# Kernel tuning notes

Hardware: AMD Instinct MI355X
Metric: run time of the kernel (lower is better)

## Reference

```python
import jax, jax.numpy as jnp
import numpy as np

N_NODES = 100000
N_EDGES = 1000000
D_NODE = 64
D_EDGE = 32
D_OUT = 64
EPS = 1e-07
BETA = 1.0


def setup_inputs() -> dict:
    key = jax.random.key(0)
    ks = jax.random.split(key, 6)
    node_feats = jax.random.normal(ks[0], (N_NODES, D_NODE), dtype=jnp.float32)
    edge_feats = jax.random.normal(ks[1], (N_EDGES, D_EDGE), dtype=jnp.float32)
    src = jax.random.randint(ks[2], (N_EDGES,), 0, N_NODES, dtype=jnp.int32)
    dst = jax.random.randint(ks[3], (N_EDGES,), 0, N_NODES, dtype=jnp.int32)
    We = jax.random.normal(ks[4], (D_EDGE, D_OUT), dtype=jnp.float32) / np.sqrt(D_EDGE)
    be = jnp.zeros((D_OUT,), dtype=jnp.float32)
    Wm = jax.random.normal(ks[5], (D_NODE, D_OUT), dtype=jnp.float32) / np.sqrt(D_NODE)
    bm = jnp.zeros((D_OUT,), dtype=jnp.float32)
    return {"node_feats": node_feats, "edge_feats": edge_feats, "src": src,
            "dst": dst, "We": We, "be": be, "Wm": Wm, "bm": bm}


def reference(node_feats, edge_feats, src, dst, We, be, Wm, bm):
    n = node_feats.shape[0]
    # edge encoder + u_add_e: m_e = h_src + Linear(e)
    m = node_feats[src] + (edge_feats @ We + be)          # [E, D]
    m = jax.nn.relu(m) + EPS
    # segmented (per-destination) softmax over edges, per feature channel
    z = m * BETA
    zmax = jax.ops.segment_max(z, dst, num_segments=n)    # [N, D]
    ez = jnp.exp(z - zmax[dst])                           # [E, D]
    denom = jax.ops.segment_sum(ez, dst, num_segments=n)  # [N, D]
    a = ez / denom[dst]                                   # [E, D]
    # weighted scatter-sum aggregation
    agg = jax.ops.segment_sum(m * a, dst, num_segments=n) # [N, D]
    feats = node_feats + agg
    # mlp_layers=1 -> single Linear
    return feats @ Wm + bm
```

## Files before the change

kernel.cpp:

```cpp
#include <hip/hip_runtime.h>

#define D_NODE 64
#define D_EDGE 32
#define D_OUT  64
#define EPSF   1e-7f
#define CAP    48
#define CHUNK  8

typedef const __attribute__((address_space(1))) unsigned int guint_t;
typedef __attribute__((address_space(3))) unsigned int luint_t;
typedef float f32x2 __attribute__((ext_vector_type(2)));

__global__ __launch_bounds__(256) void genconv_build_kernel(
    const int* __restrict__ src,
    const int* __restrict__ dst,
    int* __restrict__ cnt,
    int2* __restrict__ slots,
    int E)
{
    const int e = blockIdx.x * blockDim.x + threadIdx.x;
    if (e >= E) return;
    const int d = dst[e];
    const int pos = atomicAdd(&cnt[d], 1);
    if (pos < CAP)
        slots[d * CAP + pos] = make_int2(e, src[e]);
}

__global__ __launch_bounds__(256) void genconv_gather_kernel(
    const float* __restrict__ node,
    const float* __restrict__ ef,
    const int*  __restrict__ cnt,
    const int2* __restrict__ slots,
    const float* __restrict__ We,
    const float* __restrict__ be,
    const float* __restrict__ Wm,
    const float* __restrict__ bm,
    float* __restrict__ out,
    int N)
{
    __shared__ float wm_s[D_NODE * D_OUT];
    __shared__ __align__(16) float efs[4][2][CHUNK * D_EDGE];
    __shared__ __align__(16) float fbuf[4][D_NODE];

    for (int i = threadIdx.x; i < D_NODE * D_OUT; i += blockDim.x)
        wm_s[i] = Wm[i];
    __syncthreads();

    const int lane  = (int)(threadIdx.x & 63);
    const int wslot = (int)(threadIdx.x >> 6);
    float* const efA    = efs[wslot][0];
    float* const efB    = efs[wslot][1];
    float* const fbuf_w = fbuf[wslot];

    f32x2 w2[D_EDGE / 2];
#pragma unroll
    for (int k2 = 0; k2 < D_EDGE / 2; ++k2) {
        w2[k2][0] = We[(2 * k2 + 0) * D_OUT + lane];
        w2[k2][1] = We[(2 * k2 + 1) * D_OUT + lane];
    }
    const float bias_e = be[lane];
    const float bias_m = bm[lane];

    const int wid = (int)((blockIdx.x * blockDim.x + threadIdx.x) >> 6);
    const int nw  = (int)((gridDim.x * blockDim.x) >> 6);

    int n = wid;
    int   c_pf   = 0;
    int2  sl_pf  = make_int2(0, 0);
    float res_pf = 0.0f;
    if (n < N) {
        c_pf   = cnt[n];
        sl_pf  = (lane < CAP) ? slots[n * CAP + lane] : make_int2(0, 0);
        res_pf = node[(size_t)n * D_NODE + lane];
    }

    struct HBank { float h0, h1, h2, h3, h4, h5, h6, h7; };

    while (n < N) {
        const int c = min(c_pf, CAP);
        const int e_l = (lane < c) ? sl_pf.x : 0;
        const int s_l = (lane < c) ? sl_pf.y : 0;
        const float fres = res_pf;

        const int n_next = n + nw;
        if (n_next < N) {
            c_pf   = cnt[n_next];
            sl_pf  = (lane < CAP) ? slots[n_next * CAP + lane] : make_int2(0, 0);
            res_pf = node[(size_t)n_next * D_NODE + lane];
        }
        __builtin_amdgcn_sched_barrier(0);

        float num = 0.0f, den = 0.0f;

        auto stage = [&](int base, float* dstLDS) {
            const int r  = base + (lane >> 3);
            const int er = __builtin_amdgcn_ds_bpermute(r << 2, e_l);
            const float* g = ef + (size_t)er * D_EDGE + ((lane & 7) << 2);
            __builtin_amdgcn_global_load_lds((guint_t*)g, (luint_t*)dstLDS, 16, 0, 0);
        };
        auto hload = [&](int base, HBank& H) {
            const int s0 = __builtin_amdgcn_readlane(s_l, base + 0);
            const int s1 = __builtin_amdgcn_readlane(s_l, base + 1);
            const int s2 = __builtin_amdgcn_readlane(s_l, base + 2);
            const int s3 = __builtin_amdgcn_readlane(s_l, base + 3);
            const int s4 = __builtin_amdgcn_readlane(s_l, base + 4);
            const int s5 = __builtin_amdgcn_readlane(s_l, base + 5);
            const int s6 = __builtin_amdgcn_readlane(s_l, base + 6);
            const int s7 = __builtin_amdgcn_readlane(s_l, base + 7);
            H.h0 = node[(size_t)s0 * D_NODE + lane];
            H.h1 = node[(size_t)s1 * D_NODE + lane];
            H.h2 = node[(size_t)s2 * D_NODE + lane];
            H.h3 = node[(size_t)s3 * D_NODE + lane];
            H.h4 = node[(size_t)s4 * D_NODE + lane];
            H.h5 = node[(size_t)s5 * D_NODE + lane];
            H.h6 = node[(size_t)s6 * D_NODE + lane];
            H.h7 = node[(size_t)s7 * D_NODE + lane];
        };
        auto pairop = [&](float ha, float hb, const float* eb0, bool second_ok) {
            const float* eb1 = eb0 + D_EDGE;
            f32x2 acc0 = {0.0f, 0.0f};
            f32x2 acc1 = {0.0f, 0.0f};
#pragma unroll
            for (int k4 = 0; k4 < 8; ++k4) {
                const float4 a0 = *(const float4*)(eb0 + k4 * 4);
                const float4 a1 = *(const float4*)(eb1 + k4 * 4);
                const f32x2 wa = w2[2 * k4 + 0];
                const f32x2 wb = w2[2 * k4 + 1];
                const f32x2 p0 = {a0.x, a0.y};
                const f32x2 q0 = {a0.z, a0.w};
                const f32x2 p1 = {a1.x, a1.y};
                const f32x2 q1 = {a1.z, a1.w};
                acc0 = __builtin_elementwise_fma(p0, wa, acc0);
                acc0 = __builtin_elementwise_fma(q0, wb, acc0);
                acc1 = __builtin_elementwise_fma(p1, wa, acc1);
                acc1 = __builtin_elementwise_fma(q1, wb, acc1);
            }
            const float v0 = bias_e + acc0[0] + acc0[1];
            const float m0 = fmaxf(ha + v0, 0.0f) + EPSF;
            const float z0 = __expf(m0);
            num = fmaf(m0, z0, num);
            den += z0;
            if (second_ok) {
                const float v1 = bias_e + acc1[0] + acc1[1];
                const float m1 = fmaxf(hb + v1, 0.0f) + EPSF;
                const float z1 = __expf(m1);
                num = fmaf(m1, z1, num);
                den += z1;
            }
        };
        auto consume = [&](const float* eb, HBank& H, int base) {
            if (base + 0 < c) pairop(H.h0, H.h1, eb + 0 * D_EDGE, base + 1 < c);
            if (base + 2 < c) pairop(H.h2, H.h3, eb + 2 * D_EDGE, base + 3 < c);
            if (base + 4 < c) pairop(H.h4, H.h5, eb + 4 * D_EDGE, base + 5 < c);
            if (base + 6 < c) pairop(H.h6, H.h7, eb + 6 * D_EDGE, base + 7 < c);
        };

        const int nch = (c + CHUNK - 1) >> 3;
        if (nch > 0) {
            HBank HA, HB_;
            stage(0, efA);
            hload(0, HA);
            for (int p = 0; ; ) {
                {
                    const bool more = (p + 1 < nch);
                    if (more) { stage((p + 1) * CHUNK, efB); hload((p + 1) * CHUNK, HB_); }
                    if (more) asm volatile("s_waitcnt vmcnt(9)" ::: "memory");
                    else      asm volatile("s_waitcnt vmcnt(0)" ::: "memory");
                    __builtin_amdgcn_sched_barrier(0);
                    consume(efA, HA, p * CHUNK);
                    if (++p >= nch) break;
                }
                {
                    const bool more = (p + 1 < nch);
                    if (more) { stage((p + 1) * CHUNK, efA); hload((p + 1) * CHUNK, HA); }
                    if (more) asm volatile("s_waitcnt vmcnt(9)" ::: "memory");
                    else      asm volatile("s_waitcnt vmcnt(0)" ::: "memory");
                    __builtin_amdgcn_sched_barrier(0);
                    consume(efB, HB_, p * CHUNK);
                    if (++p >= nch) break;
                }
            }
        }

        float f = fres;
        if (c > 0)
            f += num / den;

        fbuf_w[lane] = f;
        f32x2 acc2 = {bias_m, 0.0f};
#pragma unroll
        for (int d4 = 0; d4 < D_NODE / 4; ++d4) {
            const float4 fv = *(const float4*)&fbuf_w[d4 * 4];
            const f32x2 fp = {fv.x, fv.y};
            const f32x2 fq = {fv.z, fv.w};
            const f32x2 wp = {wm_s[(d4 * 4 + 0) * D_OUT + lane],
                              wm_s[(d4 * 4 + 1) * D_OUT + lane]};
            const f32x2 wq = {wm_s[(d4 * 4 + 2) * D_OUT + lane],
                              wm_s[(d4 * 4 + 3) * D_OUT + lane]};
            acc2 = __builtin_elementwise_fma(fp, wp, acc2);
            acc2 = __builtin_elementwise_fma(fq, wq, acc2);
        }
        out[(size_t)n * D_NODE + lane] = acc2[0] + acc2[1];

        n = n_next;
    }
}

extern "C" void kernel_launch(void* const* d_in, const int* in_sizes, int n_in,
                              void* d_out, int out_size, void* d_ws, size_t ws_size,
                              hipStream_t stream)
{
    const float* node = (const float*)d_in[0];
    const float* ef   = (const float*)d_in[1];
    const int*   src  = (const int*)d_in[2];
    const int*   dst  = (const int*)d_in[3];
    const float* We   = (const float*)d_in[4];
    const float* be   = (const float*)d_in[5];
    const float* Wm   = (const float*)d_in[6];
    const float* bm   = (const float*)d_in[7];
    float* out = (float*)d_out;

    const int N = in_sizes[0] / D_NODE;
    const int E = in_sizes[2];

    int*  cnt   = (int*)d_ws;
    int2* slots = (int2*)(cnt + N);

    hipMemsetAsync(cnt, 0, (size_t)N * sizeof(int), stream);

    genconv_build_kernel<<<(E + 255) / 256, 256, 0, stream>>>(src, dst, cnt, slots, E);

    genconv_gather_kernel<<<2048, 256, 0, stream>>>(node, ef, cnt, slots,
                                                    We, be, Wm, bm, out, N);
}
```

Measured before the change: 375.2 us.

## Stage source-node rows into LDS via async global_load_lds; read Wm from global

Replaces per-lane register gathers of the eight source-node rows per chunk with two 16-byte-per-lane global_load_lds transfers into double-buffered LDS, alongside the existing edge-feature staging. The wait count drops to vmcnt(3) to match the fewer in-flight loads. The Wm shared-memory copy and its block barrier are removed, and the output projection now reads Wm from global/cache per node. The aim is to cut vector-memory instruction count and VGPR pressure in the gather pipeline. In exchange it adds LDS traffic and repeated global Wm loads in the epilogue.

```diff
diff --git a/kernel.cpp b/kernel.cpp
--- a/kernel.cpp
+++ b/kernel.cpp
@@ -38,18 +38,16 @@
     float* __restrict__ out,
     int N)
 {
-    __shared__ float wm_s[D_NODE * D_OUT];
     __shared__ __align__(16) float efs[4][2][CHUNK * D_EDGE];
+    __shared__ __align__(16) float hfs[4][2][CHUNK * D_NODE];
     __shared__ __align__(16) float fbuf[4][D_NODE];
-
-    for (int i = threadIdx.x; i < D_NODE * D_OUT; i += blockDim.x)
-        wm_s[i] = Wm[i];
-    __syncthreads();
 
     const int lane  = (int)(threadIdx.x & 63);
     const int wslot = (int)(threadIdx.x >> 6);
     float* const efA    = efs[wslot][0];
     float* const efB    = efs[wslot][1];
+    float* const hfA    = hfs[wslot][0];
+    float* const hfB    = hfs[wslot][1];
     float* const fbuf_w = fbuf[wslot];
 
     f32x2 w2[D_EDGE / 2];
@@ -74,8 +72,6 @@
         res_pf = node[(size_t)n * D_NODE + lane];
     }
 
-    struct HBank { float h0, h1, h2, h3, h4, h5, h6, h7; };
-
     while (n < N) {
         const int c = min(c_pf, CAP);
         const int e_l = (lane < c) ? sl_pf.x : 0;
@@ -92,32 +88,27 @@
 
         float num = 0.0f, den = 0.0f;
 
-        auto stage = [&](int base, float* dstLDS) {
-            const int r  = base + (lane >> 3);
-            const int er = __builtin_amdgcn_ds_bpermute(r << 2, e_l);
-            const float* g = ef + (size_t)er * D_EDGE + ((lane & 7) << 2);
-            __builtin_amdgcn_global_load_lds((guint_t*)g, (luint_t*)dstLDS, 16, 0, 0);
+        auto stage = [&](int base, float* efDst, float* hDst) {
+            const int re = base + (lane >> 3);
+            const int ee = __builtin_amdgcn_ds_bpermute(re << 2, e_l);
+            const float* ge = ef + (size_t)ee * D_EDGE + ((lane & 7) << 2);
+            __builtin_amdgcn_global_load_lds((guint_t*)ge, (luint_t*)efDst, 16, 0, 0);
+
+            const int rh0 = base + (lane >> 4);
+            const int sh0 = __builtin_amdgcn_ds_bpermute(rh0 << 2, s_l);
+            const float* gh0 = node + (size_t)sh0 * D_NODE + ((lane & 15) << 2);
+            __builtin_amdgcn_global_load_lds((guint_t*)gh0, (luint_t*)hDst, 16, 0, 0);
+
+            const int rh1 = base + 4 + (lane >> 4);
+            const int sh1 = __builtin_amdgcn_ds_bpermute(rh1 << 2, s_l);
+            const float* gh1 = node + (size_t)sh1 * D_NODE + ((lane & 15) << 2);
+            __builtin_amdgcn_global_load_lds((guint_t*)gh1, (luint_t*)(hDst + 4 * D_NODE), 16, 0, 0);
         };
-        auto hload = [&](int base, HBank& H) {
-            const int s0 = __builtin_amdgcn_readlane(s_l, base + 0);
-            const int s1 = __builtin_amdgcn_readlane(s_l, base + 1);
-            const int s2 = __builtin_amdgcn_readlane(s_l, base + 2);
-            const int s3 = __builtin_amdgcn_readlane(s_l, base + 3);
-            const int s4 = __builtin_amdgcn_readlane(s_l, base + 4);
-            const int s5 = __builtin_amdgcn_readlane(s_l, base + 5);
-            const int s6 = __builtin_amdgcn_readlane(s_l, base + 6);
-            const int s7 = __builtin_amdgcn_readlane(s_l, base + 7);
-            H.h0 = node[(size_t)s0 * D_NODE + lane];
-            H.h1 = node[(size_t)s1 * D_NODE + lane];
-            H.h2 = node[(size_t)s2 * D_NODE + lane];
-            H.h3 = node[(size_t)s3 * D_NODE + lane];
-            H.h4 = node[(size_t)s4 * D_NODE + lane];
-            H.h5 = node[(size_t)s5 * D_NODE + lane];
-            H.h6 = node[(size_t)s6 * D_NODE + lane];
-            H.h7 = node[(size_t)s7 * D_NODE + lane];
-        };
-        auto pairop = [&](float ha, float hb, const float* eb0, bool second_ok) {
+
+        auto pairop = [&](const float* hb, int t, const float* eb0, bool second_ok) {
             const float* eb1 = eb0 + D_EDGE;
+            const float ha = hb[(2 * t + 0) * D_NODE + lane];
+            const float hbv = hb[(2 * t + 1) * D_NODE + lane];
             f32x2 acc0 = {0.0f, 0.0f};
             f32x2 acc1 = {0.0f, 0.0f};
 #pragma unroll
@@ -142,41 +133,39 @@
             den += z0;
             if (second_ok) {
                 const float v1 = bias_e + acc1[0] + acc1[1];
-                const float m1 = fmaxf(hb + v1, 0.0f) + EPSF;
+                const float m1 = fmaxf(hbv + v1, 0.0f) + EPSF;
                 const float z1 = __expf(m1);
                 num = fmaf(m1, z1, num);
                 den += z1;
             }
         };
-        auto consume = [&](const float* eb, HBank& H, int base) {
-            if (base + 0 < c) pairop(H.h0, H.h1, eb + 0 * D_EDGE, base + 1 < c);
-            if (base + 2 < c) pairop(H.h2, H.h3, eb + 2 * D_EDGE, base + 3 < c);
-            if (base + 4 < c) pairop(H.h4, H.h5, eb + 4 * D_EDGE, base + 5 < c);
-            if (base + 6 < c) pairop(H.h6, H.h7, eb + 6 * D_EDGE, base + 7 < c);
+        auto consume = [&](const float* eb, const float* hb, int base) {
+            if (base + 0 < c) pairop(hb, 0, eb + 0 * D_EDGE, base + 1 < c);
+            if (base + 2 < c) pairop(hb, 1, eb + 2 * D_EDGE, base + 3 < c);
+            if (base + 4 < c) pairop(hb, 2, eb + 4 * D_EDGE, base + 5 < c);
+            if (base + 6 < c) pairop(hb, 3, eb + 6 * D_EDGE, base + 7 < c);
         };
 
         const int nch = (c + CHUNK - 1) >> 3;
         if (nch > 0) {
-            HBank HA, HB_;
-            stage(0, efA);
-            hload(0, HA);
+            stage(0, efA, hfA);
             for (int p = 0; ; ) {
                 {
                     const bool more = (p + 1 < nch);
-                    if (more) { stage((p + 1) * CHUNK, efB); hload((p + 1) * CHUNK, HB_); }
-                    if (more) asm volatile("s_waitcnt vmcnt(9)" ::: "memory");
+                    if (more) stage((p + 1) * CHUNK, efB, hfB);
+                    if (more) asm volatile("s_waitcnt vmcnt(3)" ::: "memory");
                     else      asm volatile("s_waitcnt vmcnt(0)" ::: "memory");
                     __builtin_amdgcn_sched_barrier(0);
-                    consume(efA, HA, p * CHUNK);
+                    consume(efA, hfA, p * CHUNK);
                     if (++p >= nch) break;
                 }
                 {
                     const bool more = (p + 1 < nch);
-                    if (more) { stage((p + 1) * CHUNK, efA); hload((p + 1) * CHUNK, HA); }
-                    if (more) asm volatile("s_waitcnt vmcnt(9)" ::: "memory");
+                    if (more) stage((p + 1) * CHUNK, efA, hfA);
+                    if (more) asm volatile("s_waitcnt vmcnt(3)" ::: "memory");
                     else      asm volatile("s_waitcnt vmcnt(0)" ::: "memory");
                     __builtin_amdgcn_sched_barrier(0);
-                    consume(efB, HB_, p * CHUNK);
+                    consume(efB, hfB, p * CHUNK);
                     if (++p >= nch) break;
                 }
             }
@@ -188,17 +177,26 @@
 
         fbuf_w[lane] = f;
         f32x2 acc2 = {bias_m, 0.0f};
+#pragma unroll 1
+        for (int b = 0; b < 4; ++b) {
 #pragma unroll
-        for (int d4 = 0; d4 < D_NODE / 4; ++d4) {
-            const float4 fv = *(const float4*)&fbuf_w[d4 * 4];
-            const f32x2 fp = {fv.x, fv.y};
-            const f32x2 fq = {fv.z, fv.w};
-            const f32x2 wp = {wm_s[(d4 * 4 + 0) * D_OUT + lane],
-                              wm_s[(d4 * 4 + 1) * D_OUT + lane]};
-            const f32x2 wq = {wm_s[(d4 * 4 + 2) * D_OUT + lane],
-                              wm_s[(d4 * 4 + 3) * D_OUT + lane]};
-            acc2 = __builtin_elementwise_fma(fp, wp, acc2);
-            acc2 = __builtin_elementwise_fma(fq, wq, acc2);
+            for (int q = 0; q < 2; ++q) {
+                const int d4 = b * 2 + q;
+                const float4 fv = *(const float4*)&fbuf_w[d4 * 8];
+                const float4 fv2 = *(const float4*)&fbuf_w[d4 * 8 + 4];
+                const f32x2 wp = {Wm[(d4 * 8 + 0) * D_OUT + lane],
+                                  Wm[(d4 * 8 + 1) * D_OUT + lane]};
+                const f32x2 wq = {Wm[(d4 * 8 + 2) * D_OUT + lane],
+                                  Wm[(d4 * 8 + 3) * D_OUT + lane]};
+                const f32x2 wr = {Wm[(d4 * 8 + 4) * D_OUT + lane],
+                                  Wm[(d4 * 8 + 5) * D_OUT + lane]};
+                const f32x2 ws = {Wm[(d4 * 8 + 6) * D_OUT + lane],
+                                  Wm[(d4 * 8 + 7) * D_OUT + lane]};
+                acc2 = __builtin_elementwise_fma((f32x2){fv.x,  fv.y},  wp, acc2);
+                acc2 = __builtin_elementwise_fma((f32x2){fv.z,  fv.w},  wq, acc2);
+                acc2 = __builtin_elementwise_fma((f32x2){fv2.x, fv2.y}, wr, acc2);
+                acc2 = __builtin_elementwise_fma((f32x2){fv2.z, fv2.w}, ws, acc2);
+            }
         }
         out[(size_t)n * D_NODE + lane] = acc2[0] + acc2[1];
 
```

Result: slower. 399.8 us (+6.5%).
